# Optimization experiments

Measured on AMD Instinct MI355X. Metric: run time of the kernel, lower is better.

Reference implementation:

```python
import math
import jax, jax.numpy as jnp
import numpy as np

L, T, B, C, H, DFF, K = 2, 1024, 4, 256, 4, 1024, 31
HD = C // H
EPS = 1e-5


def layer_norm(x, g, b):
    m = jnp.mean(x, axis=-1, keepdims=True)
    v = jnp.var(x, axis=-1, keepdims=True)
    return (x - m) * jax.lax.rsqrt(v + EPS) * g + b


def swish(x):
    return x * jax.nn.sigmoid(x)


def rel_shift(x):
    # x: (B, H, T, 2T-1) -> (B, H, T, T); out[..., i, j] = x[..., i, T-1-i+j]
    t = x.shape[2]
    idx = (t - 1) - jnp.arange(t)[:, None] + jnp.arange(t)[None, :]
    return jnp.take_along_axis(x, idx[None, None], axis=3)


def rel_attn(y, pos_emb, in_w, in_b, out_w, out_b, pos_w, bu, bv):
    # y: (T, B, C)
    qkv = y @ in_w.T + in_b
    q, k, v = jnp.split(qkv, 3, axis=-1)
    heads = lambda t: jnp.transpose(t.reshape(T, B, H, HD), (1, 2, 0, 3))  # (B,H,T,HD)
    scaling = HD ** -0.5
    q = heads(q) * scaling
    k = heads(k)
    v = heads(v)
    p = (pos_emb[0] @ pos_w.T).reshape(2 * T - 1, H, HD)  # (2T-1, H, HD)
    matrix_ac = jnp.einsum('bhtd,bhsd->bhts', q + bu[None, :, None, :], k)
    matrix_bd = jnp.einsum('bhtd,nhd->bhtn', q + bv[None, :, None, :], p)
    scores = matrix_ac + rel_shift(matrix_bd)  # (B,H,T,T)
    w = jax.nn.softmax(scores, axis=-1)
    o = jnp.einsum('bhts,bhsd->bhtd', w, v)
    o = jnp.transpose(o, (2, 0, 1, 3)).reshape(T, B, C)
    return o @ out_w.T + out_b


def conv_module(x, pw1_w, pw1_b, dw_w, dw_b, bn_g, bn_b, bn_m, bn_v, pw2_w, pw2_b):
    # x: (T, B, C) -> (B, C, T)
    y = jnp.transpose(x, (1, 2, 0))
    y = jnp.einsum('oc,bct->bot', pw1_w, y) + pw1_b[None, :, None]  # (B, 2C, T)
    a, g = jnp.split(y, 2, axis=1)
    y = a * jax.nn.sigmoid(g)  # GLU
    y = jax.lax.conv_general_dilated(
        y, dw_w[:, None, :], (1,), [((K - 1) // 2, (K - 1) // 2)],
        dimension_numbers=('NCH', 'OIH', 'NCH'), feature_group_count=C)
    y = y + dw_b[None, :, None]
    y = (y - bn_m[None, :, None]) * jax.lax.rsqrt(bn_v + EPS)[None, :, None] * bn_g[None, :, None] + bn_b[None, :, None]
    y = swish(y)
    y = jnp.einsum('oc,bct->bot', pw2_w, y) + pw2_b[None, :, None]
    return jnp.transpose(y, (2, 0, 1))  # (T, B, C)


def ffn(y, w1, b1, w2, b2):
    return swish(y @ w1.T + b1) @ w2.T + b2


def _forward(x, pos_emb, ffm_w1, ffm_b1, ffm_w2, ffm_b2, ff_w1, ff_b1, ff_w2, ff_b2,
             in_w, in_b, out_w, out_b, pos_w, bias_u, bias_v,
             pw1_w, pw1_b, dw_w, dw_b, bn_g, bn_b, bn_m, bn_v, pw2_w, pw2_b, ln_g, ln_b):
    for i in range(L):
        # macaron feed-forward (pre-norm, half residual)
        y = layer_norm(x, ln_g[i, 0], ln_b[i, 0])
        x = x + 0.5 * ffn(y, ffm_w1[i], ffm_b1[i], ffm_w2[i], ffm_b2[i])
        # rel-pos multi-head attention
        y = layer_norm(x, ln_g[i, 1], ln_b[i, 1])
        x = x + rel_attn(y, pos_emb, in_w[i], in_b[i], out_w[i], out_b[i], pos_w[i], bias_u[i], bias_v[i])
        # convolution module
        y = layer_norm(x, ln_g[i, 2], ln_b[i, 2])
        x = x + conv_module(y, pw1_w[i], pw1_b[i], dw_w[i], dw_b[i], bn_g[i], bn_b[i], bn_m[i], bn_v[i], pw2_w[i], pw2_b[i])
        # feed-forward (half residual)
        y = layer_norm(x, ln_g[i, 3], ln_b[i, 3])
        x = x + 0.5 * ffn(y, ff_w1[i], ff_b1[i], ff_w2[i], ff_b2[i])
        # final norm
        x = layer_norm(x, ln_g[i, 4], ln_b[i, 4])
    return x


def setup_inputs() -> dict:
    key = jax.random.key(0)
    ks = jax.random.split(key, 16)
    s = 0.02
    rn = lambda k, shape: jax.random.normal(k, shape, jnp.float32) * s
    return {
        'x': jax.random.normal(ks[0], (T, B, C), jnp.float32),
        'pos_emb': jax.random.normal(ks[1], (1, 2 * T - 1, C), jnp.float32),
        'ffm_w1': rn(ks[2], (L, DFF, C)), 'ffm_b1': jnp.zeros((L, DFF), jnp.float32),
        'ffm_w2': rn(ks[3], (L, C, DFF)), 'ffm_b2': jnp.zeros((L, C), jnp.float32),
        'ff_w1': rn(ks[4], (L, DFF, C)), 'ff_b1': jnp.zeros((L, DFF), jnp.float32),
        'ff_w2': rn(ks[5], (L, C, DFF)), 'ff_b2': jnp.zeros((L, C), jnp.float32),
        'in_w': rn(ks[6], (L, 3 * C, C)), 'in_b': jnp.zeros((L, 3 * C), jnp.float32),
        'out_w': rn(ks[7], (L, C, C)), 'out_b': jnp.zeros((L, C), jnp.float32),
        'pos_w': rn(ks[8], (L, C, C)),
        'bias_u': rn(ks[9], (L, H, HD)), 'bias_v': rn(ks[10], (L, H, HD)),
        'pw1_w': rn(ks[11], (L, 2 * C, C)), 'pw1_b': jnp.zeros((L, 2 * C), jnp.float32),
        'dw_w': rn(ks[12], (L, C, K)), 'dw_b': jnp.zeros((L, C), jnp.float32),
        'bn_g': jnp.ones((L, C), jnp.float32), 'bn_b': jnp.zeros((L, C), jnp.float32),
        'bn_m': jnp.zeros((L, C), jnp.float32), 'bn_v': jnp.ones((L, C), jnp.float32),
        'pw2_w': rn(ks[13], (L, C, C)), 'pw2_b': jnp.zeros((L, C), jnp.float32),
        'ln_g': jnp.ones((L, 5, C), jnp.float32), 'ln_b': jnp.zeros((L, 5, C), jnp.float32),
    }


def reference(x, pos_emb, ffm_w1, ffm_b1, ffm_w2, ffm_b2, ff_w1, ff_b1, ff_w2, ff_b2,
              in_w, in_b, out_w, out_b, pos_w, bias_u, bias_v,
              pw1_w, pw1_b, dw_w, dw_b, bn_g, bn_b, bn_m, bn_v, pw2_w, pw2_b, ln_g, ln_b):
    return _forward(x, pos_emb, ffm_w1, ffm_b1, ffm_w2, ffm_b2, ff_w1, ff_b1, ff_w2, ff_b2,
                    in_w, in_b, out_w, out_b, pos_w, bias_u, bias_v,
                    pw1_w, pw1_b, dw_w, dw_b, bn_g, bn_b, bn_m, bn_v, pw2_w, pw2_b, ln_g, ln_b)
```

## Files before the change

kernel.cpp:

```cpp
#include <hip/hip_runtime.h>
#include <math.h>

#define TT 1024
#define BB 4
#define CH 256
#define NH 4
#define HDIM 64
#define DFFN 1024
#define KW 31
#define NL 2
#define TB (TT*BB)
#define EPSV 1e-5f

typedef __attribute__((ext_vector_type(8))) short short8;
typedef __attribute__((ext_vector_type(4))) short short4v;
typedef __attribute__((ext_vector_type(4))) float f32x4;

__device__ __forceinline__ short f2bf(float f){
    union { float f; unsigned u; } x; x.f = f;
    unsigned r = x.u + 0x7fffu + ((x.u >> 16) & 1u);
    return (short)(r >> 16);
}

struct CvtSeg { const float* src; short* dst; int n; int mode; };
struct CvtArgs { CvtSeg seg[20]; };

__global__ __launch_bounds__(256)
void cvt_kernel(CvtArgs args)
{
    CvtSeg s = args.seg[blockIdx.y];
    int i = (blockIdx.x*256 + threadIdx.x)*8;
    if (i >= s.n) return;
    float4 a = *(const float4*)(s.src + i);
    float4 b = *(const float4*)(s.src + i + 4);
    short8 o;
    o[0]=f2bf(a.x); o[1]=f2bf(a.y); o[2]=f2bf(a.z); o[3]=f2bf(a.w);
    o[4]=f2bf(b.x); o[5]=f2bf(b.y); o[6]=f2bf(b.z); o[7]=f2bf(b.w);
    int di = i;
    if (s.mode == 1) {
        int c = i >> 8, k = i & 255;
        int dr = (c < 256) ? 2*c : 2*(c-256)+1;
        di = dr*256 + k;
    }
    *(short8*)(s.dst + di) = o;
}

template<int OUTBF>
__global__ __launch_bounds__(256)
void ln_kernel(const float* __restrict__ X, const float* __restrict__ G,
               const float* __restrict__ Bt, void* __restrict__ Y)
{
    int row  = blockIdx.x*4 + (threadIdx.x >> 6);
    int lane = threadIdx.x & 63;
    float4 v = ((const float4*)X)[(size_t)row*64 + lane];
    float s  = v.x + v.y + v.z + v.w;
    float s2 = v.x*v.x + v.y*v.y + v.z*v.z + v.w*v.w;
    #pragma unroll
    for (int off = 32; off >= 1; off >>= 1) {
        s  += __shfl_xor(s, off);
        s2 += __shfl_xor(s2, off);
    }
    float mean = s * (1.0f/CH);
    float var  = s2 * (1.0f/CH) - mean*mean;
    float inv  = rsqrtf(var + EPSV);
    float4 g4 = ((const float4*)G)[lane];
    float4 b4 = ((const float4*)Bt)[lane];
    float o0 = (v.x-mean)*inv*g4.x + b4.x;
    float o1 = (v.y-mean)*inv*g4.y + b4.y;
    float o2 = (v.z-mean)*inv*g4.z + b4.z;
    float o3 = (v.w-mean)*inv*g4.w + b4.w;
    if (OUTBF) {
        short4v o; o[0]=f2bf(o0); o[1]=f2bf(o1); o[2]=f2bf(o2); o[3]=f2bf(o3);
        *(short4v*)((short*)Y + (size_t)row*CH + lane*4) = o;
    } else {
        float4 o = {o0,o1,o2,o3};
        ((float4*)Y)[(size_t)row*64 + lane] = o;
    }
}

template<int ACT, int OUTBF, int TM>
__global__ __launch_bounds__(256)
void gemm_bf(const short* __restrict__ A, int lda, long sA,
             const short* __restrict__ Bm, int ldb, long sB,
             void* __restrict__ Cv, long ldcm, long ldcn, long sC,
             const float* __restrict__ biasM, const float* __restrict__ biasN,
             const float* __restrict__ Rm, float scale,
             int M, int N, int Kd,
             short* __restrict__ x1, short* __restrict__ x2,
             short* __restrict__ x3, short* __restrict__ x4,
             const float* __restrict__ f1, const float* __restrict__ f2)
{
    constexpr int MI = TM/32;
    __shared__ short As[2][TM][72];
    __shared__ short Bs[2][64][72];
    const int bz = blockIdx.z;
    A  += (long)bz * sA;
    Bm += (long)bz * sB;
    const int m0 = blockIdx.y * TM;
    const int n0 = blockIdx.x * 64;
    const int tid = threadIdx.x;
    const int w = tid >> 6, lane = tid & 63;
    const int g = lane >> 4, c = lane & 15;
    const int wr = w >> 1, wc = w & 1;
    const int srow = tid >> 3, scol = (tid & 7) * 8;

    const short *Ap[MI], *Bp[2];
    #pragma unroll
    for (int p = 0; p < MI; ++p) {
        int gm = m0 + srow + p*32; if (gm >= M) gm = M - 1;
        Ap[p] = A + (long)gm*lda + scol;
    }
    #pragma unroll
    for (int p = 0; p < 2; ++p) {
        int gn = n0 + srow + p*32; if (gn >= N) gn = N - 1;
        Bp[p] = Bm + (long)gn*ldb + scol;
    }

    const int niter = Kd >> 6;
    short8 raA[MI], raB[MI], rbA[2], rbB[2];
    #pragma unroll
    for (int p = 0; p < MI; ++p) { raA[p] = *(const short8*)(Ap[p]); raB[p] = *(const short8*)(Ap[p] + 64); }
    #pragma unroll
    for (int p = 0; p < 2;  ++p) { rbA[p] = *(const short8*)(Bp[p]); rbB[p] = *(const short8*)(Bp[p] + 64); }

    f32x4 acc[MI][2] = {};
    auto do_mfma = [&](int bufc) {
        #pragma unroll
        for (int ks = 0; ks < 2; ++ks) {
            short8 af[MI], bfr[2];
            #pragma unroll
            for (int i = 0; i < MI; ++i) af[i]  = *(const short8*)&As[bufc][wr*(TM/2) + i*16 + c][ks*32 + 8*g];
            #pragma unroll
            for (int j = 0; j < 2; ++j)  bfr[j] = *(const short8*)&Bs[bufc][wc*32 + j*16 + c][ks*32 + 8*g];
            #pragma unroll
            for (int i = 0; i < MI; ++i)
                #pragma unroll
                for (int j = 0; j < 2; ++j)
                    acc[i][j] = __builtin_amdgcn_mfma_f32_16x16x32_bf16(af[i], bfr[j], acc[i][j], 0,0,0);
        }
    };

    for (int it = 0; it < niter; it += 2) {
        #pragma unroll
        for (int p = 0; p < MI; ++p) *(short8*)&As[0][srow + p*32][scol] = raA[p];
        #pragma unroll
        for (int p = 0; p < 2;  ++p) *(short8*)&Bs[0][srow + p*32][scol] = rbA[p];
        __syncthreads();
        if (it + 2 < niter) {
            int kt2 = (it+2) << 6;
            #pragma unroll
            for (int p = 0; p < MI; ++p) raA[p] = *(const short8*)(Ap[p] + kt2);
            #pragma unroll
            for (int p = 0; p < 2;  ++p) rbA[p] = *(const short8*)(Bp[p] + kt2);
        }
        do_mfma(0);
        #pragma unroll
        for (int p = 0; p < MI; ++p) *(short8*)&As[1][srow + p*32][scol] = raB[p];
        #pragma unroll
        for (int p = 0; p < 2;  ++p) *(short8*)&Bs[1][srow + p*32][scol] = rbB[p];
        __syncthreads();
        if (it + 3 < niter) {
            int kt3 = (it+3) << 6;
            #pragma unroll
            for (int p = 0; p < MI; ++p) raB[p] = *(const short8*)(Ap[p] + kt3);
            #pragma unroll
            for (int p = 0; p < 2;  ++p) rbB[p] = *(const short8*)(Bp[p] + kt3);
        }
        do_mfma(1);
    }

    if (ACT == 3) {
        const int region = n0 >> 8;
        #pragma unroll
        for (int i = 0; i < MI; ++i)
            #pragma unroll
            for (int r = 0; r < 4; ++r) {
                int m = m0 + wr*(TM/2) + i*16 + 4*g + r;
                int t = m >> 2, b = m & 3;
                #pragma unroll
                for (int j = 0; j < 2; ++j) {
                    int n = n0 + wc*32 + j*16 + c;
                    float v = acc[i][j][r] + biasN[n];
                    int h = (n >> 6) & 3, d = n & 63;
                    int bh = b*NH + h;
                    if (region == 0) {
                        float q = v * 0.125f;
                        size_t di = ((size_t)bh*TT + t)*HDIM + d;
                        x1[di] = f2bf(q + f1[h*HDIM + d]);
                        x2[di] = f2bf(q + f2[h*HDIM + d]);
                    } else if (region == 1) {
                        x3[((size_t)bh*TT + t)*HDIM + d] = f2bf(v);
                    } else {
                        x4[((size_t)bh*HDIM + d)*TT + t] = f2bf(v);
                    }
                }
            }
        return;
    }
    if (ACT == 4) {
        #pragma unroll
        for (int i = 0; i < MI; ++i)
            #pragma unroll
            for (int r = 0; r < 4; ++r) {
                int m = m0 + wr*(TM/2) + i*16 + 4*g + r;
                if (m >= M) continue;
                #pragma unroll
                for (int j = 0; j < 2; ++j) {
                    int n = n0 + wc*32 + j*16 + c;
                    int h = n >> 6, d = n & 63;
                    x1[((size_t)h*2048 + m)*HDIM + d] = f2bf(acc[i][j][r]);
                }
            }
        return;
    }
    if (ACT == 2) {
        float* Cf = (float*)Cv + (long)bz*sC;
        #pragma unroll
        for (int i = 0; i < MI; ++i)
            #pragma unroll
            for (int rp = 0; rp < 2; ++rp) {
                int ma = m0 + wr*(TM/2) + i*16 + 4*g + 2*rp;
                float va = acc[i][0][2*rp]   + biasM[ma>>1];
                float vg = acc[i][0][2*rp+1] + biasM[(ma>>1)+CH];
                float vb = acc[i][1][2*rp]   + biasM[ma>>1];
                float hg = acc[i][1][2*rp+1] + biasM[(ma>>1)+CH];
                #pragma unroll
                for (int j = 0; j < 2; ++j) {
                    int n = n0 + wc*32 + j*16 + c;
                    float a = j ? vb : va;
                    float gg = j ? hg : vg;
                    Cf[(long)(ma>>1)*ldcm + n] = a / (1.f + __expf(-gg));
                }
            }
        return;
    }

    #pragma unroll
    for (int i = 0; i < MI; ++i) {
        #pragma unroll
        for (int r = 0; r < 4; ++r) {
            int m = m0 + wr*(TM/2) + i*16 + 4*g + r;
            if (m >= M) continue;
            float bm = biasM ? biasM[m] : 0.f;
            #pragma unroll
            for (int j = 0; j < 2; ++j) {
                int n = n0 + wc*32 + j*16 + c;
                if (n >= N) continue;
                float v = acc[i][j][r] + bm + (biasN ? biasN[n] : 0.f);
                if (ACT == 1) v = v / (1.f + __expf(-v));
                v *= scale;
                long ci = (long)m*ldcm + (long)n*ldcn;
                if (OUTBF) {
                    ((short*)Cv)[(long)bz*sC + ci] = f2bf(v);
                } else {
                    float* Cf = (float*)Cv + (long)bz*sC;
                    if (Rm) v += (Rm + (long)bz*sC)[ci];
                    Cf[ci] = v;
                }
            }
        }
    }
}

__global__ __launch_bounds__(256)
void attn_mfma_kernel(const short* __restrict__ qub, const short* __restrict__ qvb,
                      const short* __restrict__ kb, const short* __restrict__ vtb,
                      const short* __restrict__ pbf, short* __restrict__ O)
{
    const int t0 = blockIdx.x * 64;
    const int h  = blockIdx.y, b = blockIdx.z;
    const int bh = b*NH + h;
    const int tid = threadIdx.x;
    const int w = tid >> 6, lane = tid & 63;
    const int g = lane >> 4, c = lane & 15;

    __shared__ short Kl[64][88];
    __shared__ short Pl[128][88];
    __shared__ float BDs[4][16][84];
    __shared__ short Pa[4][16][88];

    short8 qa[2], qv[2];
    {
        const short* qr = qub + ((size_t)bh*TT + t0 + 16*w + c)*HDIM;
        const short* vr = qvb + ((size_t)bh*TT + t0 + 16*w + c)*HDIM;
        qa[0] = *(const short8*)(qr + 8*g);
        qa[1] = *(const short8*)(qr + 32 + 8*g);
        qv[0] = *(const short8*)(vr + 8*g);
        qv[1] = *(const short8*)(vr + 32 + 8*g);
    }

    const short* ksrc = kb  + (size_t)bh*TT*HDIM + tid*8;
    const short* psrc = pbf + ((size_t)h*2048 + (960 - t0))*HDIM + tid*8;
    const short* vbase = vtb + ((size_t)bh*HDIM)*TT;

    short8 rk0, rk1, rp0, rp1, rp2, rp3;
    {
        rk0 = *(const short8*)(ksrc);
        rk1 = *(const short8*)(ksrc + 2048);
        rp0 = *(const short8*)(psrc);
        rp1 = *(const short8*)(psrc + 2048);
        rp2 = *(const short8*)(psrc + 4096);
        rp3 = *(const short8*)(psrc + 6144);
    }

    f32x4 acc_o[4] = {};
    float m_run[4], l_run[4];
    #pragma unroll
    for (int r = 0; r < 4; ++r){ m_run[r] = -1e30f; l_run[r] = 0.f; }

    for (int jt = 0; jt < 16; ++jt) {
        const int j0 = jt*64;
        {
            int ci0 = tid, ci1 = tid + 256;
            *(short8*)&Kl[ci0>>3][(ci0&7)*8] = rk0;
            *(short8*)&Kl[ci1>>3][(ci1&7)*8] = rk1;
            *(short8*)&Pl[(ci0>>3)     ][(ci0&7)*8] = rp0;
            *(short8*)&Pl[(ci1>>3)     ][(ci1&7)*8] = rp1;
            *(short8*)&Pl[(ci0>>3) + 64][(ci0&7)*8] = rp2;
            *(short8*)&Pl[(ci1>>3) + 64][(ci1&7)*8] = rp3;
        }
        __syncthreads();
        short8 vfr[2][4];
        #pragma unroll
        for (int ks = 0; ks < 2; ++ks)
            #pragma unroll
            for (int df = 0; df < 4; ++df)
                vfr[ks][df] = *(const short8*)(vbase + (size_t)(df*16 + c)*TT + j0 + ks*32 + 8*g);
        if (jt < 15) {
            int j0n = (jt+1)*64;
            rk0 = *(const short8*)(ksrc + (size_t)j0n*HDIM);
            rk1 = *(const short8*)(ksrc + (size_t)j0n*HDIM + 2048);
            rp0 = *(const short8*)(psrc + (size_t)j0n*HDIM);
            rp1 = *(const short8*)(psrc + (size_t)j0n*HDIM + 2048);
            rp2 = *(const short8*)(psrc + (size_t)j0n*HDIM + 4096);
            rp3 = *(const short8*)(psrc + (size_t)j0n*HDIM + 6144);
        }

        f32x4 acc_s[4] = {};
        #pragma unroll
        for (int ks = 0; ks < 2; ++ks)
            #pragma unroll
            for (int jf = 0; jf < 4; ++jf) {
                short8 bf = *(const short8*)&Kl[jf*16 + c][ks*32 + 8*g];
                acc_s[jf] = __builtin_amdgcn_mfma_f32_16x16x32_bf16(qa[ks], bf, acc_s[jf], 0,0,0);
            }
        f32x4 acc_b[5] = {};
        #pragma unroll
        for (int ks = 0; ks < 2; ++ks)
            #pragma unroll
            for (int fi = 0; fi < 5; ++fi) {
                short8 bf = *(const short8*)&Pl[(3-w+fi)*16 + c][ks*32 + 8*g];
                acc_b[fi] = __builtin_amdgcn_mfma_f32_16x16x32_bf16(qv[ks], bf, acc_b[fi], 0,0,0);
            }
        #pragma unroll
        for (int fi = 0; fi < 5; ++fi)
            #pragma unroll
            for (int r = 0; r < 4; ++r)
                BDs[w][4*g + r][16*fi + c] = acc_b[fi][r];

        float rmax[4];
        #pragma unroll
        for (int r = 0; r < 4; ++r) rmax[r] = -1e30f;
        #pragma unroll
        for (int jf = 0; jf < 4; ++jf)
            #pragma unroll
            for (int r = 0; r < 4; ++r) {
                int row = 4*g + r;
                float s = acc_s[jf][r] + BDs[w][row][15 - row + 16*jf + c];
                acc_s[jf][r] = s;
                rmax[r] = fmaxf(rmax[r], s);
            }
        #pragma unroll
        for (int r = 0; r < 4; ++r)
            #pragma unroll
            for (int msk = 1; msk < 16; msk <<= 1)
                rmax[r] = fmaxf(rmax[r], __shfl_xor(rmax[r], msk));
        float fs[4], rsum[4];
        #pragma unroll
        for (int r = 0; r < 4; ++r) {
            float mn = fmaxf(m_run[r], rmax[r]);
            fs[r] = __expf(m_run[r] - mn);
            m_run[r] = mn;
            rsum[r] = 0.f;
        }
        #pragma unroll
        for (int jf = 0; jf < 4; ++jf)
            #pragma unroll
            for (int r = 0; r < 4; ++r) {
                float p = __expf(acc_s[jf][r] - m_run[r]);
                rsum[r] += p;
                Pa[w][4*g + r][16*jf + c] = f2bf(p);
            }
        #pragma unroll
        for (int r = 0; r < 4; ++r) {
            #pragma unroll
            for (int msk = 1; msk < 16; msk <<= 1)
                rsum[r] += __shfl_xor(rsum[r], msk);
            l_run[r] = l_run[r]*fs[r] + rsum[r];
        }
        #pragma unroll
        for (int df = 0; df < 4; ++df)
            #pragma unroll
            for (int r = 0; r < 4; ++r)
                acc_o[df][r] *= fs[r];

        #pragma unroll
        for (int ks = 0; ks < 2; ++ks) {
            short8 pa = *(const short8*)&Pa[w][c][ks*32 + 8*g];
            #pragma unroll
            for (int df = 0; df < 4; ++df)
                acc_o[df] = __builtin_amdgcn_mfma_f32_16x16x32_bf16(pa, vfr[ks][df], acc_o[df], 0,0,0);
        }
        __syncthreads();
    }

    #pragma unroll
    for (int df = 0; df < 4; ++df)
        #pragma unroll
        for (int r = 0; r < 4; ++r) {
            int t = t0 + 16*w + 4*g + r;
            O[((size_t)t*BB + b)*CH + h*HDIM + 16*df + c] = f2bf(acc_o[df][r] / l_run[r]);
        }
}

__global__ __launch_bounds__(256)
void dwconv_kernel(const float* __restrict__ In,
                   const float* __restrict__ W,
                   const float* __restrict__ CB,
                   const float* __restrict__ BNG, const float* __restrict__ BNB,
                   const float* __restrict__ BNM, const float* __restrict__ BNV,
                   short* __restrict__ Out)
{
    int c = blockIdx.x, b = blockIdx.y;
    __shared__ float row[TT + KW - 1];
    __shared__ float wv[KW];
    int tid = threadIdx.x;
    const float* base = In + ((size_t)b*CH + c)*TT;
    for (int i = tid; i < TT + KW - 1; i += 256) {
        int tp = i - (KW-1)/2;
        row[i] = (tp >= 0 && tp < TT) ? base[tp] : 0.f;
    }
    if (tid < KW) wv[tid] = W[c*KW + tid];
    float bias = CB[c];
    float scl  = rsqrtf(BNV[c] + EPSV) * BNG[c];
    float sh   = BNB[c];
    float mn   = BNM[c];
    __syncthreads();
    #pragma unroll
    for (int r = 0; r < 4; ++r) {
        int t = tid + 256*r;
        float acc = 0.f;
        #pragma unroll
        for (int k = 0; k < KW; ++k) acc += row[t + k] * wv[k];
        float v = (acc + bias - mn) * scl + sh;
        v = v / (1.f + __expf(-v));
        Out[((size_t)t*BB + b)*CH + c] = f2bf(v);
    }
}

extern "C" void kernel_launch(void* const* d_in, const int* in_sizes, int n_in,
                              void* d_out, int out_size, void* d_ws, size_t ws_size,
                              hipStream_t stream)
{
    const float* x_in    = (const float*)d_in[0];
    const float* pos_emb = (const float*)d_in[1];
    const float* ffm_w1  = (const float*)d_in[2];
    const float* ffm_b1  = (const float*)d_in[3];
    const float* ffm_w2  = (const float*)d_in[4];
    const float* ffm_b2  = (const float*)d_in[5];
    const float* ff_w1   = (const float*)d_in[6];
    const float* ff_b1   = (const float*)d_in[7];
    const float* ff_w2   = (const float*)d_in[8];
    const float* ff_b2   = (const float*)d_in[9];
    const float* in_w    = (const float*)d_in[10];
    const float* in_b    = (const float*)d_in[11];
    const float* out_w   = (const float*)d_in[12];
    const float* out_b   = (const float*)d_in[13];
    const float* pos_w   = (const float*)d_in[14];
    const float* bias_u  = (const float*)d_in[15];
    const float* bias_v  = (const float*)d_in[16];
    const float* pw1_w   = (const float*)d_in[17];
    const float* pw1_b   = (const float*)d_in[18];
    const float* dw_w    = (const float*)d_in[19];
    const float* dw_b    = (const float*)d_in[20];
    const float* bn_g    = (const float*)d_in[21];
    const float* bn_b    = (const float*)d_in[22];
    const float* bn_m    = (const float*)d_in[23];
    const float* bn_v    = (const float*)d_in[24];
    const float* pw2_w   = (const float*)d_in[25];
    const float* pw2_b   = (const float*)d_in[26];
    const float* ln_g    = (const float*)d_in[27];
    const float* ln_b    = (const float*)d_in[28];

    char* wp = (char*)d_ws;
    auto alloc = [&](size_t bytes) -> void* {
        void* p = wp; wp += (bytes + 255) & ~(size_t)255; return p;
    };
    float* xbuf = (float*)alloc((size_t)TB*CH*4);
    short* ybf  = (short*)alloc((size_t)TB*CH*2);
    short* hff  = (short*)alloc((size_t)TB*DFFN*2);
    float* c2   = (float*)alloc((size_t)BB*CH*TT*4);
    short* abf  = (short*)alloc((size_t)TB*CH*2);
    short* qub  = (short*)alloc((size_t)BB*NH*TT*HDIM*2);
    short* qvb  = (short*)alloc((size_t)BB*NH*TT*HDIM*2);
    short* kb   = (short*)alloc((size_t)BB*NH*TT*HDIM*2);
    short* vtb  = (short*)alloc((size_t)BB*NH*TT*HDIM*2);
    short* pbb  = (short*)alloc((size_t)NH*2048*HDIM*2);
    short* wbf[NL][9];
    int    wn[9] = { DFFN*CH, CH*DFFN, DFFN*CH, CH*DFFN, 3*CH*CH, CH*CH, CH*CH, 2*CH*CH, CH*CH };
    const float* wsrc[NL][9];
    for (int i = 0; i < NL; ++i) {
        const float* srcs[9] = {
            ffm_w1 + (size_t)i*DFFN*CH, ffm_w2 + (size_t)i*CH*DFFN,
            ff_w1  + (size_t)i*DFFN*CH, ff_w2  + (size_t)i*CH*DFFN,
            in_w   + (size_t)i*3*CH*CH, out_w  + (size_t)i*CH*CH,
            pos_w  + (size_t)i*CH*CH,   pw1_w  + (size_t)i*2*CH*CH,
            pw2_w  + (size_t)i*CH*CH };
        for (int j = 0; j < 9; ++j) {
            wsrc[i][j] = srcs[j];
            wbf[i][j]  = (short*)alloc((size_t)wn[j]*2);
        }
    }
    short* posbf = (short*)alloc((size_t)(2*TT-1)*CH*2);
    if ((size_t)(wp - (char*)d_ws) > ws_size) return;

    hipMemsetAsync(pbb, 0, (size_t)NH*2048*HDIM*2, stream);

    CvtArgs ca;
    int nseg = 0, maxn = 0;
    for (int i = 0; i < NL; ++i)
        for (int j = 0; j < 9; ++j) {
            ca.seg[nseg++] = { wsrc[i][j], wbf[i][j], wn[j], (j == 7) ? 1 : 0 };
            if (wn[j] > maxn) maxn = wn[j];
        }
    ca.seg[nseg++] = { pos_emb, posbf, (2*TT-1)*CH, 0 };
    if ((2*TT-1)*CH > maxn) maxn = (2*TT-1)*CH;
    cvt_kernel<<<dim3((maxn/8 + 255)/256, nseg), 256, 0, stream>>>(ca);

    const float* cur = x_in;
    for (int i = 0; i < NL; ++i) {
        const float* lng = ln_g + (size_t)i*5*CH;
        const float* lnb = ln_b + (size_t)i*5*CH;

        ln_kernel<1><<<TB/4, 256, 0, stream>>>(cur, lng + 0*CH, lnb + 0*CH, ybf);
        gemm_bf<1,1,64><<<dim3(DFFN/64, TB/64), 256, 0, stream>>>(
            ybf, CH, 0, wbf[i][0], CH, 0, hff, DFFN, 1, 0,
            nullptr, ffm_b1 + (size_t)i*DFFN, nullptr, 1.f, TB, DFFN, CH,
            nullptr,nullptr,nullptr,nullptr,nullptr,nullptr);
        gemm_bf<0,0,32><<<dim3(CH/64, TB/32), 256, 0, stream>>>(
            hff, DFFN, 0, wbf[i][1], DFFN, 0, xbuf, CH, 1, 0,
            nullptr, ffm_b2 + (size_t)i*CH, cur, 0.5f, TB, CH, DFFN,
            nullptr,nullptr,nullptr,nullptr,nullptr,nullptr);
        cur = xbuf;

        ln_kernel<1><<<TB/4, 256, 0, stream>>>(cur, lng + 1*CH, lnb + 1*CH, ybf);
        gemm_bf<3,1,64><<<dim3(3*CH/64, TB/64), 256, 0, stream>>>(
            ybf, CH, 0, wbf[i][4], CH, 0, nullptr, 0, 0, 0,
            nullptr, in_b + (size_t)i*3*CH, nullptr, 1.f, TB, 3*CH, CH,
            qub, qvb, kb, vtb,
            bias_u + (size_t)i*NH*HDIM, bias_v + (size_t)i*NH*HDIM);
        gemm_bf<4,1,64><<<dim3(CH/64, (2*TT-1+63)/64), 256, 0, stream>>>(
            posbf, CH, 0, wbf[i][6], CH, 0, nullptr, 0, 0, 0,
            nullptr, nullptr, nullptr, 1.f, 2*TT-1, CH, CH,
            pbb, nullptr, nullptr, nullptr, nullptr, nullptr);
        attn_mfma_kernel<<<dim3(TT/64, NH, BB), 256, 0, stream>>>(
            qub, qvb, kb, vtb, pbb, abf);
        gemm_bf<0,0,32><<<dim3(CH/64, TB/32), 256, 0, stream>>>(
            abf, CH, 0, wbf[i][5], CH, 0, xbuf, CH, 1, 0,
            nullptr, out_b + (size_t)i*CH, cur, 1.f, TB, CH, CH,
            nullptr,nullptr,nullptr,nullptr,nullptr,nullptr);

        ln_kernel<1><<<TB/4, 256, 0, stream>>>(cur, lng + 2*CH, lnb + 2*CH, ybf);
        gemm_bf<2,0,64><<<dim3(TT/64, (2*CH)/64, BB), 256, 0, stream>>>(
            wbf[i][7], CH, 0, ybf, BB*CH, CH, c2, TT, 1, (long)CH*TT,
            pw1_b + (size_t)i*2*CH, nullptr, nullptr, 1.f, 2*CH, TT, CH,
            nullptr,nullptr,nullptr,nullptr,nullptr,nullptr);
        dwconv_kernel<<<dim3(CH, BB), 256, 0, stream>>>(
            c2, dw_w + (size_t)i*CH*KW, dw_b + (size_t)i*CH,
            bn_g + (size_t)i*CH, bn_b + (size_t)i*CH,
            bn_m + (size_t)i*CH, bn_v + (size_t)i*CH, abf);
        gemm_bf<0,0,32><<<dim3(CH/64, TB/32), 256, 0, stream>>>(
            abf, CH, 0, wbf[i][8], CH, 0, xbuf, CH, 1, 0,
            nullptr, pw2_b + (size_t)i*CH, cur, 1.f, TB, CH, CH,
            nullptr,nullptr,nullptr,nullptr,nullptr,nullptr);

        ln_kernel<1><<<TB/4, 256, 0, stream>>>(cur, lng + 3*CH, lnb + 3*CH, ybf);
        gemm_bf<1,1,64><<<dim3(DFFN/64, TB/64), 256, 0, stream>>>(
            ybf, CH, 0, wbf[i][2], CH, 0, hff, DFFN, 1, 0,
            nullptr, ff_b1 + (size_t)i*DFFN, nullptr, 1.f, TB, DFFN, CH,
            nullptr,nullptr,nullptr,nullptr,nullptr,nullptr);
        gemm_bf<0,0,32><<<dim3(CH/64, TB/32), 256, 0, stream>>>(
            hff, DFFN, 0, wbf[i][3], DFFN, 0, xbuf, CH, 1, 0,
            nullptr, ff_b2 + (size_t)i*CH, cur, 0.5f, TB, CH, DFFN,
            nullptr,nullptr,nullptr,nullptr,nullptr,nullptr);

        if (i == NL-1)
            ln_kernel<0><<<TB/4, 256, 0, stream>>>(xbuf, lng + 4*CH, lnb + 4*CH, (float*)d_out);
        else
            ln_kernel<0><<<TB/4, 256, 0, stream>>>(xbuf, lng + 4*CH, lnb + 4*CH, xbuf);
        cur = xbuf;
    }
}
```

Measured before the change: 414.2 us.

## Split attention over two key halves with combine kernel; store GLU output as bf16

The attention kernel now splits the key range into two halves across blockIdx.z, doubling the grid from 256 to 512 blocks. Each half writes unnormalized fp32 partial outputs plus running max and sum, and a new combine kernel merges them flash-decoding style into bf16. Separately, the GLU epilogue of the pw1 GEMM now writes bf16 instead of fp32, and the depthwise conv reads bf16, halving that intermediate's memory traffic. The costs are an extra kernel launch, an fp32 partial buffer round trip, and some precision loss on the GLU output.

```diff
diff --git a/kernel.cpp b/kernel.cpp
--- a/kernel.cpp
+++ b/kernel.cpp
@@ -20,6 +20,9 @@
     union { float f; unsigned u; } x; x.f = f;
     unsigned r = x.u + 0x7fffu + ((x.u >> 16) & 1u);
     return (short)(r >> 16);
+}
+__device__ __forceinline__ float bf2f(short s){
+    union { unsigned u; float f; } x; x.u = ((unsigned)(unsigned short)s) << 16; return x.f;
 }
 
 struct CvtSeg { const float* src; short* dst; int n; int mode; };
@@ -214,7 +217,7 @@
         return;
     }
     if (ACT == 2) {
-        float* Cf = (float*)Cv + (long)bz*sC;
+        short* Cs = (short*)Cv + (long)bz*sC;
         #pragma unroll
         for (int i = 0; i < MI; ++i)
             #pragma unroll
@@ -229,7 +232,7 @@
                     int n = n0 + wc*32 + j*16 + c;
                     float a = j ? vb : va;
                     float gg = j ? hg : vg;
-                    Cf[(long)(ma>>1)*ldcm + n] = a / (1.f + __expf(-gg));
+                    Cs[(long)(ma>>1)*ldcm + n] = f2bf(a / (1.f + __expf(-gg)));
                 }
             }
         return;
@@ -265,14 +268,17 @@
 __global__ __launch_bounds__(256)
 void attn_mfma_kernel(const short* __restrict__ qub, const short* __restrict__ qvb,
                       const short* __restrict__ kb, const short* __restrict__ vtb,
-                      const short* __restrict__ pbf, short* __restrict__ O)
+                      const short* __restrict__ pbf,
+                      float* __restrict__ Opart, float2* __restrict__ ml)
 {
     const int t0 = blockIdx.x * 64;
-    const int h  = blockIdx.y, b = blockIdx.z;
+    const int h  = blockIdx.y;
+    const int b  = blockIdx.z >> 1, s = blockIdx.z & 1;
     const int bh = b*NH + h;
     const int tid = threadIdx.x;
     const int w = tid >> 6, lane = tid & 63;
     const int g = lane >> 4, c = lane & 15;
+    const int jt0 = s*8, jt1 = jt0 + 8;
 
     __shared__ short Kl[64][88];
     __shared__ short Pl[128][88];
@@ -295,12 +301,13 @@
 
     short8 rk0, rk1, rp0, rp1, rp2, rp3;
     {
-        rk0 = *(const short8*)(ksrc);
-        rk1 = *(const short8*)(ksrc + 2048);
-        rp0 = *(const short8*)(psrc);
-        rp1 = *(const short8*)(psrc + 2048);
-        rp2 = *(const short8*)(psrc + 4096);
-        rp3 = *(const short8*)(psrc + 6144);
+        size_t o0 = (size_t)(jt0*64)*HDIM;
+        rk0 = *(const short8*)(ksrc + o0);
+        rk1 = *(const short8*)(ksrc + o0 + 2048);
+        rp0 = *(const short8*)(psrc + o0);
+        rp1 = *(const short8*)(psrc + o0 + 2048);
+        rp2 = *(const short8*)(psrc + o0 + 4096);
+        rp3 = *(const short8*)(psrc + o0 + 6144);
     }
 
     f32x4 acc_o[4] = {};
@@ -308,7 +315,7 @@
     #pragma unroll
     for (int r = 0; r < 4; ++r){ m_run[r] = -1e30f; l_run[r] = 0.f; }
 
-    for (int jt = 0; jt < 16; ++jt) {
+    for (int jt = jt0; jt < jt1; ++jt) {
         const int j0 = jt*64;
         {
             int ci0 = tid, ci1 = tid + 256;
@@ -326,14 +333,14 @@
             #pragma unroll
             for (int df = 0; df < 4; ++df)
                 vfr[ks][df] = *(const short8*)(vbase + (size_t)(df*16 + c)*TT + j0 + ks*32 + 8*g);
-        if (jt < 15) {
-            int j0n = (jt+1)*64;
-            rk0 = *(const short8*)(ksrc + (size_t)j0n*HDIM);
-            rk1 = *(const short8*)(ksrc + (size_t)j0n*HDIM + 2048);
-            rp0 = *(const short8*)(psrc + (size_t)j0n*HDIM);
-            rp1 = *(const short8*)(psrc + (size_t)j0n*HDIM + 2048);
-            rp2 = *(const short8*)(psrc + (size_t)j0n*HDIM + 4096);
-            rp3 = *(const short8*)(psrc + (size_t)j0n*HDIM + 6144);
+        if (jt + 1 < jt1) {
+            size_t on = (size_t)((jt+1)*64)*HDIM;
+            rk0 = *(const short8*)(ksrc + on);
+            rk1 = *(const short8*)(ksrc + on + 2048);
+            rp0 = *(const short8*)(psrc + on);
+            rp1 = *(const short8*)(psrc + on + 2048);
+            rp2 = *(const short8*)(psrc + on + 4096);
+            rp3 = *(const short8*)(psrc + on + 6144);
         }
 
         f32x4 acc_s[4] = {};
@@ -366,9 +373,9 @@
             #pragma unroll
             for (int r = 0; r < 4; ++r) {
                 int row = 4*g + r;
-                float s = acc_s[jf][r] + BDs[w][row][15 - row + 16*jf + c];
-                acc_s[jf][r] = s;
-                rmax[r] = fmaxf(rmax[r], s);
+                float sc = acc_s[jf][r] + BDs[w][row][15 - row + 16*jf + c];
+                acc_s[jf][r] = sc;
+                rmax[r] = fmaxf(rmax[r], sc);
             }
         #pragma unroll
         for (int r = 0; r < 4; ++r)
@@ -419,12 +426,45 @@
         #pragma unroll
         for (int r = 0; r < 4; ++r) {
             int t = t0 + 16*w + 4*g + r;
-            O[((size_t)t*BB + b)*CH + h*HDIM + 16*df + c] = f2bf(acc_o[df][r] / l_run[r]);
-        }
+            Opart[(((size_t)s*16 + bh)*TT + t)*HDIM + 16*df + c] = acc_o[df][r];
+        }
+    if (c == 0) {
+        #pragma unroll
+        for (int r = 0; r < 4; ++r) {
+            int t = t0 + 16*w + 4*g + r;
+            float2 v; v.x = m_run[r]; v.y = l_run[r];
+            ml[((size_t)s*16 + bh)*TT + t] = v;
+        }
+    }
 }
 
 __global__ __launch_bounds__(256)
-void dwconv_kernel(const float* __restrict__ In,
+void attn_combine_kernel(const float* __restrict__ Opart, const float2* __restrict__ ml,
+                         short* __restrict__ O)
+{
+    int idx = blockIdx.x*256 + threadIdx.x;
+    int base = idx*4;
+    int d = base & 63;
+    int t = (base >> 6) & (TT-1);
+    int bh = base >> 16;
+    float2 a  = ml[(size_t)bh*TT + t];
+    float2 b2 = ml[(size_t)(16 + bh)*TT + t];
+    float m = fmaxf(a.x, b2.x);
+    float w1 = __expf(a.x - m), w2 = __expf(b2.x - m);
+    float inv = 1.f / (w1*a.y + w2*b2.y);
+    float4 o1 = ((const float4*)Opart)[idx];
+    float4 o2 = ((const float4*)(Opart + (1<<20)))[idx];
+    int b = bh >> 2, h = bh & 3;
+    short4v o;
+    o[0] = f2bf((w1*o1.x + w2*o2.x) * inv);
+    o[1] = f2bf((w1*o1.y + w2*o2.y) * inv);
+    o[2] = f2bf((w1*o1.z + w2*o2.z) * inv);
+    o[3] = f2bf((w1*o1.w + w2*o2.w) * inv);
+    *(short4v*)(O + ((size_t)t*BB + b)*CH + h*HDIM + d) = o;
+}
+
+__global__ __launch_bounds__(256)
+void dwconv_kernel(const short* __restrict__ In,
                    const float* __restrict__ W,
                    const float* __restrict__ CB,
                    const float* __restrict__ BNG, const float* __restrict__ BNB,
@@ -435,10 +475,10 @@
     __shared__ float row[TT + KW - 1];
     __shared__ float wv[KW];
     int tid = threadIdx.x;
-    const float* base = In + ((size_t)b*CH + c)*TT;
+    const short* base = In + ((size_t)b*CH + c)*TT;
     for (int i = tid; i < TT + KW - 1; i += 256) {
         int tp = i - (KW-1)/2;
-        row[i] = (tp >= 0 && tp < TT) ? base[tp] : 0.f;
+        row[i] = (tp >= 0 && tp < TT) ? bf2f(base[tp]) : 0.f;
     }
     if (tid < KW) wv[tid] = W[c*KW + tid];
     float bias = CB[c];
@@ -496,16 +536,18 @@
     auto alloc = [&](size_t bytes) -> void* {
         void* p = wp; wp += (bytes + 255) & ~(size_t)255; return p;
     };
-    float* xbuf = (float*)alloc((size_t)TB*CH*4);
-    short* ybf  = (short*)alloc((size_t)TB*CH*2);
-    short* hff  = (short*)alloc((size_t)TB*DFFN*2);
-    float* c2   = (float*)alloc((size_t)BB*CH*TT*4);
-    short* abf  = (short*)alloc((size_t)TB*CH*2);
-    short* qub  = (short*)alloc((size_t)BB*NH*TT*HDIM*2);
-    short* qvb  = (short*)alloc((size_t)BB*NH*TT*HDIM*2);
-    short* kb   = (short*)alloc((size_t)BB*NH*TT*HDIM*2);
-    short* vtb  = (short*)alloc((size_t)BB*NH*TT*HDIM*2);
-    short* pbb  = (short*)alloc((size_t)NH*2048*HDIM*2);
+    float* xbuf  = (float*)alloc((size_t)TB*CH*4);
+    short* ybf   = (short*)alloc((size_t)TB*CH*2);
+    short* hff   = (short*)alloc((size_t)TB*DFFN*2);
+    short* c2    = (short*)alloc((size_t)BB*CH*TT*2);
+    short* abf   = (short*)alloc((size_t)TB*CH*2);
+    short* qub   = (short*)alloc((size_t)BB*NH*TT*HDIM*2);
+    short* qvb   = (short*)alloc((size_t)BB*NH*TT*HDIM*2);
+    short* kb    = (short*)alloc((size_t)BB*NH*TT*HDIM*2);
+    short* vtb   = (short*)alloc((size_t)BB*NH*TT*HDIM*2);
+    short* pbb   = (short*)alloc((size_t)NH*2048*HDIM*2);
+    float* opart = (float*)alloc((size_t)2*BB*NH*TT*HDIM*4);
+    float2* mlb  = (float2*)alloc((size_t)2*BB*NH*TT*8);
     short* wbf[NL][9];
     int    wn[9] = { DFFN*CH, CH*DFFN, DFFN*CH, CH*DFFN, 3*CH*CH, CH*CH, CH*CH, 2*CH*CH, CH*CH };
     const float* wsrc[NL][9];
@@ -563,15 +605,16 @@
             posbf, CH, 0, wbf[i][6], CH, 0, nullptr, 0, 0, 0,
             nullptr, nullptr, nullptr, 1.f, 2*TT-1, CH, CH,
             pbb, nullptr, nullptr, nullptr, nullptr, nullptr);
-        attn_mfma_kernel<<<dim3(TT/64, NH, BB), 256, 0, stream>>>(
-            qub, qvb, kb, vtb, pbb, abf);
+        attn_mfma_kernel<<<dim3(TT/64, NH, BB*2), 256, 0, stream>>>(
+            qub, qvb, kb, vtb, pbb, opart, mlb);
+        attn_combine_kernel<<<(BB*NH*TT*HDIM)/1024, 256, 0, stream>>>(opart, mlb, abf);
         gemm_bf<0,0,32><<<dim3(CH/64, TB/32), 256, 0, stream>>>(
             abf, CH, 0, wbf[i][5], CH, 0, xbuf, CH, 1, 0,
             nullptr, out_b + (size_t)i*CH, cur, 1.f, TB, CH, CH,
             nullptr,nullptr,nullptr,nullptr,nullptr,nullptr);
 
         ln_kernel<1><<<TB/4, 256, 0, stream>>>(cur, lng + 2*CH, lnb + 2*CH, ybf);
-        gemm_bf<2,0,64><<<dim3(TT/64, (2*CH)/64, BB), 256, 0, stream>>>(
+        gemm_bf<2,1,64><<<dim3(TT/64, (2*CH)/64, BB), 256, 0, stream>>>(
             wbf[i][7], CH, 0, ybf, BB*CH, CH, c2, TT, 1, (long)CH*TT,
             pw1_b + (size_t)i*2*CH, nullptr, nullptr, 1.f, 2*CH, TT, CH,
             nullptr,nullptr,nullptr,nullptr,nullptr,nullptr);
```

Result: no change. 414.2 us (+0.0%).
